# Optimization experiments

Hardware: AMD Instinct MI355X
Metric: run time of the kernel (lower is better)

Reference implementation:

```python
import jax, jax.numpy as jnp
import numpy as np
import math

B, S, D_MODEL = 2, 2048, 1024
H = 16
DK = D_MODEL // H          # 64, down-proj per-stream dim
NOPE, ROPE = 128, 64
D_HEAD = NOPE + ROPE       # 192 = d_latent // H
D_LATENT = H * D_HEAD      # 3072
ROT_DIM = 2 * ((ROPE // 2) // 2)  # rotary dim actually rotated = qk_rope_dim//2 = 32
EPS = 1e-6


def _rmsnorm(x, w):
    out = x * jax.lax.rsqrt(jnp.mean(x * x, axis=-1, keepdims=True) + EPS)
    return out * w


def _apply_rope(x):
    # x: [b, h, s, d]; rotate first ROT_DIM channels, interleaved pairing
    s = x.shape[-2]
    inv_freq = 1.0 / (10000.0 ** (jnp.arange(0, ROT_DIM, 2, dtype=jnp.float32) / ROT_DIM))
    freqs = jnp.arange(s, dtype=jnp.float32)[:, None] * inv_freq[None, :]  # [s, ROT_DIM//2]
    freqs = jnp.repeat(freqs, 2, axis=-1)  # [s, ROT_DIM], (f0,f0,f1,f1,...)
    cos, sin = jnp.cos(freqs), jnp.sin(freqs)
    xl, xr = x[..., :ROT_DIM], x[..., ROT_DIM:]
    x1, x2 = xl[..., 0::2], xl[..., 1::2]
    rot = jnp.stack([-x2, x1], axis=-1).reshape(xl.shape)
    xl = xl * cos + rot * sin
    return jnp.concatenate([xl, xr], axis=-1)


def setup_inputs() -> dict:
    key = jax.random.key(0)
    ks = jax.random.split(key, 5)
    sc = 0.02
    x = jax.random.normal(ks[0], (B, S, D_MODEL), jnp.float32)
    mask = jnp.broadcast_to(jnp.tril(jnp.ones((S, S), jnp.int32)), (B, S, S))
    w_down = jax.random.normal(ks[1], (D_MODEL, 3 * DK), jnp.float32) * sc
    rms_w = jnp.ones((3 * DK,), jnp.float32)
    w_up = jax.random.normal(ks[2], (3 * DK, 3 * D_LATENT), jnp.float32) * sc
    w_o = jax.random.normal(ks[3], (D_LATENT, D_MODEL), jnp.float32) * sc
    return {"x": x, "mask": mask, "w_down": w_down, "rms_w": rms_w, "w_up": w_up, "w_o": w_o}


def reference(x, mask, w_down, rms_w, w_up, w_o):
    h = x @ w_down                        # [b, s, 3*dk]
    h = _rmsnorm(h, rms_w)
    qkv = h @ w_up                        # [b, s, 3*d_latent]
    q, k, v = jnp.split(qkv, 3, axis=-1)  # each [b, s, d_latent]

    def to_heads(t):
        # einops '(d h)': d outer, h inner
        return t.reshape(B, S, D_HEAD, H).transpose(0, 3, 1, 2)  # [b, h, s, d]

    q, k, v = to_heads(q), to_heads(k), to_heads(v)
    q_nope, q_rope = q[..., :NOPE], q[..., NOPE:]
    k_nope, k_rope = k[..., :NOPE], k[..., NOPE:]
    q_rope = _apply_rope(q_rope)
    k_rope = _apply_rope(k_rope)

    scores = (jnp.einsum('bhid,bhjd->bhij', q_nope, k_nope)
              + jnp.einsum('bhid,bhjd->bhij', q_rope, k_rope))
    scores = scores / math.sqrt(NOPE + ROPE)
    scores = jnp.where(mask[:, None] == 0, -1e9, scores)
    attn = jax.nn.softmax(scores, axis=-1)

    out = jnp.einsum('bhij,bhjd->bhid', attn, v)        # [b, h, s, d]
    out = out.transpose(0, 2, 1, 3).reshape(B, S, D_LATENT)  # 'b h s d -> b s (h d)'
    return out @ w_o
```

## Files before the change

kernel.cpp:

```cpp
#include <hip/hip_runtime.h>
#include <stdint.h>
#include <stddef.h>


typedef __bf16 bf16x8 __attribute__((ext_vector_type(8)));
typedef float  f32x4  __attribute__((ext_vector_type(4)));

#define MFMA16x16(a,b,c) __builtin_amdgcn_mfma_f32_16x16x32_bf16((a),(b),(c),0,0,0)

__device__ __forceinline__ uint16_t f2bf(float f){
  union { float f; uint32_t u; } v; v.f = f;
  uint32_t u = v.u + 0x7fffu + ((v.u >> 16) & 1u);
  return (uint16_t)(u >> 16);
}
__device__ __forceinline__ bf16x8 load_frag(const uint16_t* p){
  uint4 u = *reinterpret_cast<const uint4*>(p);
  return __builtin_bit_cast(bf16x8, u);
}
__device__ __forceinline__ f32x4 fzero(){
  f32x4 z = {0.f, 0.f, 0.f, 0.f};
  return z;
}
__device__ __forceinline__ uint32_t pack2(float a, float b){
  return (uint32_t)f2bf(a) | ((uint32_t)f2bf(b) << 16);
}
__device__ __forceinline__ void gl2lds16(const uint16_t* g, uint16_t* l){
  __builtin_amdgcn_global_load_lds(
      (const __attribute__((address_space(1))) uint32_t*)g,
      (__attribute__((address_space(3))) uint32_t*)l,
      16, 0, 0);
}

__global__ __launch_bounds__(256) void k_transpose_cvt(const float* __restrict__ in,
                                                       uint16_t* __restrict__ out,
                                                       int R, int C){
  __shared__ float t[32][33];
  const int tc = blockIdx.x * 32;
  const int tr = blockIdx.y * 32;
  const int j = threadIdx.x & 31, i0 = threadIdx.x >> 5;
  for(int ii = 0; ii < 4; ++ii){
    int r = i0 + ii * 8;
    t[r][j] = in[(size_t)(tr + r) * C + tc + j];
  }
  __syncthreads();
  for(int ii = 0; ii < 4; ++ii){
    int c = i0 + ii * 8;
    out[(size_t)(tc + c) * R + tr + j] = f2bf(t[j][c]);
  }
}

__global__ __launch_bounds__(256) void k_down_mfma(const float* __restrict__ x,
                                                   const uint16_t* __restrict__ wdt,
                                                   const float* __restrict__ rms_w,
                                                   uint16_t* __restrict__ h_out){
  __shared__ __align__(16) uint16_t as[32 * 64];
  __shared__ float hsq[32];
  const int tid  = threadIdx.x;
  const int wave = tid >> 6, lane = tid & 63;
  const int ml = lane & 15, qd = lane >> 4;
  const int m0 = blockIdx.x * 32;
  const int n0w = wave * 48;
  if(tid < 32) hsq[tid] = 0.f;

  f32x4 acc[2][3];
#pragma unroll
  for(int mt = 0; mt < 2; ++mt)
#pragma unroll
    for(int nt = 0; nt < 3; ++nt) acc[mt][nt] = fzero();

  const int srow = tid >> 3, sc = tid & 7;
  for(int kt = 0; kt < 16; ++kt){
    const float* src = x + (size_t)(m0 + srow) * 1024 + kt * 64 + sc * 8;
    float4 a = *reinterpret_cast<const float4*>(src);
    float4 b = *reinterpret_cast<const float4*>(src + 4);
    uint4 pk;
    pk.x = pack2(a.x, a.y); pk.y = pack2(a.z, a.w);
    pk.z = pack2(b.x, b.y); pk.w = pack2(b.z, b.w);
    __syncthreads();
    *reinterpret_cast<uint4*>(as + srow * 64 + ((sc ^ (srow & 7)) * 8)) = pk;
    __syncthreads();
#pragma unroll
    for(int kk = 0; kk < 2; ++kk){
      bf16x8 af[2];
#pragma unroll
      for(int mt = 0; mt < 2; ++mt){
        int row = mt * 16 + ml;
        af[mt] = load_frag(as + row * 64 + (((kk * 4 + qd) ^ (row & 7)) * 8));
      }
#pragma unroll
      for(int nt = 0; nt < 3; ++nt){
        bf16x8 bfr = load_frag(wdt + (size_t)(n0w + nt * 16 + ml) * 1024 + kt * 64 + kk * 32 + qd * 8);
#pragma unroll
        for(int mt = 0; mt < 2; ++mt)
          acc[mt][nt] = MFMA16x16(af[mt], bfr, acc[mt][nt]);
      }
    }
  }
  __syncthreads();
#pragma unroll
  for(int mt = 0; mt < 2; ++mt)
#pragma unroll
    for(int r = 0; r < 4; ++r){
      float s = acc[mt][0][r]*acc[mt][0][r] + acc[mt][1][r]*acc[mt][1][r] + acc[mt][2][r]*acc[mt][2][r];
#pragma unroll
      for(int off = 1; off < 16; off <<= 1) s += __shfl_xor(s, off);
      if(ml == 0) atomicAdd(&hsq[mt * 16 + qd * 4 + r], s);
    }
  __syncthreads();
  float rw[3];
#pragma unroll
  for(int nt = 0; nt < 3; ++nt) rw[nt] = rms_w[n0w + nt * 16 + ml];
#pragma unroll
  for(int mt = 0; mt < 2; ++mt)
#pragma unroll
    for(int r = 0; r < 4; ++r){
      int row = mt * 16 + qd * 4 + r;
      float scl = rsqrtf(hsq[row] * (1.0f / 192.0f) + 1e-6f);
#pragma unroll
      for(int nt = 0; nt < 3; ++nt)
        h_out[(size_t)(m0 + row) * 192 + n0w + nt * 16 + ml] = f2bf(acc[mt][nt][r] * scl * rw[nt]);
    }
}

__global__ __launch_bounds__(256) void k_gemm_up(const uint16_t* __restrict__ hmat,
                                                 const uint16_t* __restrict__ wt,
                                                 uint16_t* __restrict__ q_t,
                                                 uint16_t* __restrict__ k_t,
                                                 uint16_t* __restrict__ v_t){
  __shared__ __align__(16) uint16_t rp[16 * 129 * 8];
  const int wave = threadIdx.x >> 6, lane = threadIdx.x & 63;
  const int ml = lane & 15, qd = lane >> 4;
  const int m0 = blockIdx.y * 32;
  const int bx = blockIdx.x;
  const int which = bx / 6;
  const int d0b = (bx % 6) * 32;
  const int n0w = bx * 512 + wave * 128;
  const int d0w = d0b + wave * 8;

  bf16x8 af[2][6];
#pragma unroll
  for(int mt = 0; mt < 2; ++mt)
#pragma unroll
    for(int kk = 0; kk < 6; ++kk)
      af[mt][kk] = load_frag(hmat + (size_t)(m0 + mt * 16 + ml) * 192 + kk * 32 + qd * 8);

  f32x4 acc[8][2];
#pragma unroll
  for(int nt = 0; nt < 8; ++nt){ acc[nt][0] = fzero(); acc[nt][1] = fzero(); }
#pragma unroll
  for(int nt = 0; nt < 8; ++nt){
#pragma unroll
    for(int kk = 0; kk < 6; ++kk){
      bf16x8 b = load_frag(wt + (size_t)(n0w + nt * 16 + ml) * 192 + kk * 32 + qd * 8);
      acc[nt][0] = MFMA16x16(af[0][kk], b, acc[nt][0]);
      acc[nt][1] = MFMA16x16(af[1][kk], b, acc[nt][1]);
    }
  }

  const int b   = m0 >> 11;
  const int s0  = m0 & 2047;
  const int kt2 = s0 >> 6;
  const int row0 = s0 & 63;
  uint4* rp4 = (uint4*)rp;

  if(which < 2){
    const float qs = which ? 1.0f : 0.07216878364870322f;
    const bool rope = (d0w >= 128) && (d0w < 160);
#pragma unroll
    for(int mt = 0; mt < 2; ++mt)
#pragma unroll
      for(int r = 0; r < 4; ++r){
        int t = mt * 16 + qd * 4 + r;
        int s = s0 + t;
        float v[8];
#pragma unroll
        for(int nt = 0; nt < 8; ++nt) v[nt] = acc[nt][mt][r] * qs;
        if(rope){
#pragma unroll
          for(int pi = 0; pi < 4; ++pi){
            int fi = (d0w + 2 * pi - 128) >> 1;
            float invf = __expf(-(float)fi * 0.5756462732485114f);
            float sn, cs;
            sincosf((float)s * invf, &sn, &cs);
            float e = v[2 * pi], o = v[2 * pi + 1];
            v[2 * pi]     = e * cs - o * sn;
            v[2 * pi + 1] = o * cs + e * sn;
          }
        }
        uint4 pk;
        pk.x = pack2(v[0], v[1]); pk.y = pack2(v[2], v[3]);
        pk.z = pack2(v[4], v[5]); pk.w = pack2(v[6], v[7]);
        rp4[ml * 129 + t * 4 + (wave ^ (t & 3))] = pk;
      }
  } else {
#pragma unroll
    for(int nt = 0; nt < 8; ++nt){
      int dl = wave * 8 + nt;
#pragma unroll
      for(int mt = 0; mt < 2; ++mt){
        int jc = mt * 2 + (qd >> 1);
        int slot = ml * 129 + dl * 4 + (jc ^ (dl & 3));
        uint2 pk;
        pk.x = pack2(acc[nt][mt][0], acc[nt][mt][1]);
        pk.y = pack2(acc[nt][mt][2], acc[nt][mt][3]);
        *(reinterpret_cast<uint2*>(rp + slot * 8) + (qd & 1)) = pk;
      }
    }
  }
  __syncthreads();

  if(which < 2){
    uint16_t* dst = which ? k_t : q_t;
    const int cb = d0b >> 3;
#pragma unroll
    for(int it = 0; it < 8; ++it){
      int h = wave * 4 + (it & 3), rhalf = it >> 2;
      int tloc = rhalf * 16 + (lane >> 2), p = lane & 3;
      int row = row0 + tloc;
      uint4 val = rp4[h * 129 + tloc * 4 + p];
      size_t off = ((size_t)(b * 16 + h) * 32 + kt2) * 12288
                 + (size_t)row * 192 + ((cb ^ (tloc & 4)) + p) * 8;
      *reinterpret_cast<uint4*>(dst + off) = val;
    }
  } else {
    const int cs0 = row0 >> 3;
#pragma unroll
    for(int it = 0; it < 8; ++it){
      int h = wave * 4 + (it & 3), dhalf = it >> 2;
      int dl = dhalf * 16 + (lane >> 2), p = lane & 3;
      uint4 val = rp4[h * 129 + dl * 4 + p];
      size_t off = ((size_t)(b * 16 + h) * 32 + kt2) * 12288
                 + (size_t)(d0b + dl) * 64 + ((cs0 ^ (dl & 4)) + p) * 8;
      *reinterpret_cast<uint4*>(v_t + off) = val;
    }
  }
}

__global__ __launch_bounds__(256, 4) void k_attn(const uint16_t* __restrict__ q_t,
                                                 const uint16_t* __restrict__ k_t,
                                                 const uint16_t* __restrict__ v_t,
                                                 uint16_t* __restrict__ attn_out){
  __shared__ __align__(16) uint16_t smem[15360];
  const int tid  = threadIdx.x;
  const int wave = tid >> 6;
  const int lane = tid & 63;
  const int ml   = lane & 15;
  const int qd   = lane >> 4;
  const int bx   = blockIdx.x;
  const int bh   = bx & 31;
  const int qt   = 31 - (bx >> 5);
  const int last = 2 * qt + 1;

  uint16_t* const kb  = smem;
  uint16_t* const vb  = smem + 6144;
  uint16_t* const psw = smem + 12800 + wave * 640;

  const uint16_t* kbase = k_t + (size_t)bh * 393216;
  const uint16_t* vbase = v_t + (size_t)bh * 393216;
  const uint16_t* qtile = q_t + (size_t)bh * 393216 + (size_t)qt * 12288;
  const int hh = bh & 15, bb = bh >> 4;

  const int c_  = (lane & 3) ^ ((lane >> 3) & 3);
  const int s7_ = (lane >> 2) & 7;
  const int vg_ = (lane >> 2) * 64;
  const int voff0 = vg_ + (((0 + c_) ^ s7_) * 8);
  const int voff1 = vg_ + (((4 + c_) ^ s7_) * 8);
  const int vpo = ml * 32 + ((qd ^ ((ml >> 1) & 3)) * 8);

#pragma unroll
  for(int it = 0; it < 6; ++it){
    int seg = wave * 6 + it;
    gl2lds16(qtile + seg * 512 + lane * 8, smem + seg * 512);
  }
  __builtin_amdgcn_sched_barrier(0);
  asm volatile("s_waitcnt vmcnt(0)" ::: "memory");
  __builtin_amdgcn_sched_barrier(0);
  __builtin_amdgcn_s_barrier();

  bf16x8 qf[6];
  {
    int row = wave * 16 + ml;
#pragma unroll
    for(int kk = 0; kk < 6; ++kk)
      qf[kk] = load_frag(smem + row * 192 + (((kk * 4 + qd) ^ (row & 7)) * 8));
  }
  ((uint32_t*)(vb + 6144))[tid] = 0x3F803F80u;
  asm volatile("s_waitcnt lgkmcnt(0)" ::: "memory");
  __builtin_amdgcn_sched_barrier(0);
  __builtin_amdgcn_s_barrier();

  auto stageKV = [&](int kt){
    const uint16_t* ksrc = kbase + (size_t)(kt >> 1) * 12288 + (kt & 1) * 6144
                         + wave * 1536 + lane * 8;
    uint16_t* kd = kb + wave * 1536;
    gl2lds16(ksrc,        kd);
    gl2lds16(ksrc + 512,  kd + 512);
    gl2lds16(ksrc + 1024, kd + 1024);
    const int vo = (kt & 1) ? voff1 : voff0;
    const uint16_t* vsrc = vbase + (size_t)(kt >> 1) * 12288 + (size_t)(wave * 3) * 1024 + vo;
    uint16_t* vd = vb + wave * 1536;
    gl2lds16(vsrc,        vd);
    gl2lds16(vsrc + 1024, vd + 512);
    gl2lds16(vsrc + 2048, vd + 1024);
  };

  stageKV(0);

  f32x4 o[13];
#pragma unroll
  for(int i = 0; i < 13; ++i) o[i] = fzero();

  const int r0 = qt * 64 + wave * 16;
  for(int kt = 0; kt <= last; ++kt){
    __builtin_amdgcn_sched_barrier(0);
    asm volatile("s_waitcnt vmcnt(0)" ::: "memory");
    __builtin_amdgcn_sched_barrier(0);
    __builtin_amdgcn_s_barrier();

    const int kl = kt * 32;
    if(kl <= r0 + 15){
      float pp[2][4];
      __builtin_amdgcn_s_setprio(1);
#pragma unroll
      for(int nt = 0; nt < 2; ++nt){
        f32x4 a = fzero();
        int row = nt * 16 + ml;
#pragma unroll
        for(int kk = 0; kk < 6; ++kk){
          bf16x8 bfr = load_frag(kb + row * 192 + (((kk * 4 + qd) ^ (row & 7)) * 8));
          a = MFMA16x16(qf[kk], bfr, a);
        }
#pragma unroll
        for(int r = 0; r < 4; ++r) pp[nt][r] = a[r];
      }
      __builtin_amdgcn_s_setprio(0);
      const bool diag = (kl + 31 > r0);
#pragma unroll
      for(int nt = 0; nt < 2; ++nt)
#pragma unroll
        for(int r = 0; r < 4; ++r){
          float v = pp[nt][r];
          if(diag){
            int i = r0 + qd * 4 + r;
            int j = kl + nt * 16 + ml;
            if(j > i) v = -1e9f;
          }
          pp[nt][r] = __expf(v);
        }
#pragma unroll
      for(int nt = 0; nt < 2; ++nt)
#pragma unroll
        for(int r = 0; r < 4; ++r)
          psw[(qd * 4 + r) * 40 + nt * 16 + ml] = f2bf(pp[nt][r]);
      bf16x8 pa = load_frag(psw + ml * 40 + qd * 8);
      __builtin_amdgcn_s_setprio(1);
#pragma unroll
      for(int dt = 0; dt < 13; ++dt){
        bf16x8 vbf = load_frag(vb + dt * 512 + vpo);
        o[dt] = MFMA16x16(pa, vbf, o[dt]);
      }
      __builtin_amdgcn_s_setprio(0);
    }
    __builtin_amdgcn_s_barrier();
    if(kt < last) stageKV(kt + 1);
  }

#pragma unroll
  for(int r = 0; r < 4; ++r){
    int i = r0 + qd * 4 + r;
    float inv = 1.0f / o[12][r];
    size_t obase = ((size_t)bb * 2048 + i) * 3072 + hh * 192;
#pragma unroll
    for(int dt = 0; dt < 12; ++dt)
      attn_out[obase + dt * 16 + ml] = f2bf(o[dt][r] * inv);
  }
}

__global__ __launch_bounds__(256) void k_gemm_o_tile(const uint16_t* __restrict__ a,
                                                     const uint16_t* __restrict__ wt,
                                                     float* __restrict__ part){
  __shared__ __align__(16) uint16_t as[128 * 64];
  __shared__ __align__(16) uint16_t bs[128 * 64];
  const int wave = threadIdx.x >> 6, lane = threadIdx.x & 63;
  const int ml = lane & 15, qd = lane >> 4;
  const int m0 = blockIdx.y * 128, n0 = blockIdx.x * 128;
  const int kz = blockIdx.z;
  const int mo = (wave >> 1) * 64, no = (wave & 1) * 64;

  const int lrow = lane >> 3;
  const int gch  = (lane & 7) ^ (lrow & 7);
  const uint16_t* abase = a  + (size_t)(m0 + lrow) * 3072 + kz * 1536 + gch * 8;
  const uint16_t* bbase = wt + (size_t)(n0 + lrow) * 3072 + kz * 1536 + gch * 8;

  f32x4 acc[4][4];
#pragma unroll
  for(int mt = 0; mt < 4; ++mt)
#pragma unroll
    for(int nt = 0; nt < 4; ++nt) acc[mt][nt] = fzero();

  for(int kt = 0; kt < 24; ++kt){
    __syncthreads();
#pragma unroll
    for(int it = 0; it < 4; ++it){
      int seg = it * 4 + wave;
      gl2lds16(abase + (size_t)seg * 24576 + kt * 64, as + seg * 512);
      gl2lds16(bbase + (size_t)seg * 24576 + kt * 64, bs + seg * 512);
    }
    __syncthreads();
#pragma unroll
    for(int ks2 = 0; ks2 < 2; ++ks2){
      bf16x8 af[4], bfr[4];
#pragma unroll
      for(int mt = 0; mt < 4; ++mt){
        int row = mo + mt * 16 + ml;
        af[mt] = load_frag(as + row * 64 + (((ks2 * 4 + qd) ^ (row & 7)) * 8));
      }
#pragma unroll
      for(int nt = 0; nt < 4; ++nt){
        int row = no + nt * 16 + ml;
        bfr[nt] = load_frag(bs + row * 64 + (((ks2 * 4 + qd) ^ (row & 7)) * 8));
      }
#pragma unroll
      for(int mt = 0; mt < 4; ++mt)
#pragma unroll
        for(int nt = 0; nt < 4; ++nt)
          acc[mt][nt] = MFMA16x16(af[mt], bfr[nt], acc[mt][nt]);
    }
  }

  float* dst = part + (size_t)kz * 4096 * 1024;
#pragma unroll
  for(int mt = 0; mt < 4; ++mt)
#pragma unroll
    for(int nt = 0; nt < 4; ++nt)
#pragma unroll
      for(int r = 0; r < 4; ++r){
        int row = m0 + mo + mt * 16 + qd * 4 + r;
        int col = n0 + no + nt * 16 + ml;
        dst[(size_t)row * 1024 + col] = acc[mt][nt][r];
      }
}

__global__ __launch_bounds__(256) void k_addout(const float* __restrict__ part,
                                                float* __restrict__ out){
  int i = blockIdx.x * 256 + threadIdx.x;
  const float4* p0 = (const float4*)part;
  const float4* p1 = p0 + (size_t)1048576;
  float4 a = p0[i], b = p1[i];
  float4 c; c.x = a.x + b.x; c.y = a.y + b.y; c.z = a.z + b.z; c.w = a.w + b.w;
  ((float4*)out)[i] = c;
}


extern "C" void kernel_launch(void* const* d_in, const int* in_sizes, int n_in,
                              void* d_out, int out_size, void* d_ws, size_t ws_size,
                              hipStream_t stream) {
  (void)in_sizes; (void)n_in; (void)out_size; (void)ws_size;
  const float* x      = (const float*)d_in[0];
  const float* w_down = (const float*)d_in[2];
  const float* rms_w  = (const float*)d_in[3];
  const float* w_up   = (const float*)d_in[4];
  const float* w_o    = (const float*)d_in[5];
  float* out = (float*)d_out;

  char* ws = (char*)d_ws;
  uint16_t* h_bf   = (uint16_t*)(ws);
  uint16_t* w_up_t = (uint16_t*)(ws + 1572864);
  uint16_t* w_o_t  = (uint16_t*)(ws + 5111808);
  uint16_t* w_dn_t = (uint16_t*)(ws + 11403264);
  uint16_t* q_tb   = (uint16_t*)(ws + 11796480);
  uint16_t* k_tb   = (uint16_t*)(ws + 36962304);
  uint16_t* v_tb   = (uint16_t*)(ws + 62128128);
  uint16_t* attnO  = (uint16_t*)(ws + 87293952);
  float*    part   = (float*)(ws + 11796480);

  k_transpose_cvt<<<dim3(288, 6), 256, 0, stream>>>(w_up, w_up_t, 192, 9216);
  k_transpose_cvt<<<dim3(32, 96), 256, 0, stream>>>(w_o,  w_o_t,  3072, 1024);
  k_transpose_cvt<<<dim3(6, 32),  256, 0, stream>>>(w_down, w_dn_t, 1024, 192);
  k_down_mfma<<<128, 256, 0, stream>>>(x, w_dn_t, rms_w, h_bf);
  k_gemm_up<<<dim3(18, 128), 256, 0, stream>>>(h_bf, w_up_t, q_tb, k_tb, v_tb);
  k_attn<<<1024, 256, 0, stream>>>(q_tb, k_tb, v_tb, attnO);
  k_gemm_o_tile<<<dim3(8, 32, 2), 256, 0, stream>>>(attnO, w_o_t, part);
  k_addout<<<4096, 256, 0, stream>>>(part, out);
}
```

Before: 350.2 us.

## Process two query tiles per attention block with double-buffered K/V staging

Each attention block now handles 128 query rows (two 64-row tiles) instead of 64, so every K/V tile staged into LDS feeds both Q tiles and K/V global traffic is halved. K/V buffers are double-buffered so the next tile's load is issued before computing on the current one, overlapping memory with MFMA work. Q fragments are loaded straight from global into registers, and blocks are ordered to pair heavy and light causal rows. In exchange, register use roughly doubles for accumulators (occupancy hint lowered to 2 blocks), grid size halves to 512 blocks, and LDS use doubles.

New measurement: 375.1 us. 1.07x slower.

```diff
diff --git a/kernel.cpp b/kernel.cpp
--- a/kernel.cpp
+++ b/kernel.cpp
@@ -236,11 +236,11 @@
   }
 }
 
-__global__ __launch_bounds__(256, 4) void k_attn(const uint16_t* __restrict__ q_t,
+__global__ __launch_bounds__(256, 2) void k_attn(const uint16_t* __restrict__ q_t,
                                                  const uint16_t* __restrict__ k_t,
                                                  const uint16_t* __restrict__ v_t,
                                                  uint16_t* __restrict__ attn_out){
-  __shared__ __align__(16) uint16_t smem[15360];
+  __shared__ __align__(16) uint16_t smem[30720];
   const int tid  = threadIdx.x;
   const int wave = tid >> 6;
   const int lane = tid & 63;
@@ -248,131 +248,150 @@
   const int qd   = lane >> 4;
   const int bx   = blockIdx.x;
   const int bh   = bx & 31;
-  const int qt   = 31 - (bx >> 5);
-  const int last = 2 * qt + 1;
-
-  uint16_t* const kb  = smem;
-  uint16_t* const vb  = smem + 6144;
-  uint16_t* const psw = smem + 12800 + wave * 640;
+  const int qb   = (bx < 256) ? (15 - (bx >> 5)) : ((bx >> 5) - 8);
+  const int last = 4 * qb + 3;
+
+  uint16_t* const kb0 = smem;
+  uint16_t* const kb1 = smem + 6144;
+  uint16_t* const vb0 = smem + 12288;
+  uint16_t* const vb1 = smem + 18944;
+  uint16_t* const psw = smem + 25600 + wave * 1280;
 
   const uint16_t* kbase = k_t + (size_t)bh * 393216;
   const uint16_t* vbase = v_t + (size_t)bh * 393216;
-  const uint16_t* qtile = q_t + (size_t)bh * 393216 + (size_t)qt * 12288;
   const int hh = bh & 15, bb = bh >> 4;
 
   const int c_  = (lane & 3) ^ ((lane >> 3) & 3);
   const int s7_ = (lane >> 2) & 7;
   const int vg_ = (lane >> 2) * 64;
-  const int voff0 = vg_ + (((0 + c_) ^ s7_) * 8);
+  const int voff0 = vg_ + ((c_ ^ s7_) * 8);
   const int voff1 = vg_ + (((4 + c_) ^ s7_) * 8);
   const int vpo = ml * 32 + ((qd ^ ((ml >> 1) & 3)) * 8);
 
-#pragma unroll
-  for(int it = 0; it < 6; ++it){
-    int seg = wave * 6 + it;
-    gl2lds16(qtile + seg * 512 + lane * 8, smem + seg * 512);
+  bf16x8 qf[2][6];
+  {
+    const int row = wave * 16 + ml;
+    const int sw = row & 7;
+#pragma unroll
+    for(int t = 0; t < 2; ++t){
+      const uint16_t* qtb = q_t + ((size_t)bh * 32 + qb * 2 + t) * 12288 + (size_t)row * 192;
+#pragma unroll
+      for(int kk = 0; kk < 6; ++kk)
+        qf[t][kk] = load_frag(qtb + (((kk * 4 + qd) ^ sw) * 8));
+    }
   }
   __builtin_amdgcn_sched_barrier(0);
   asm volatile("s_waitcnt vmcnt(0)" ::: "memory");
   __builtin_amdgcn_sched_barrier(0);
-  __builtin_amdgcn_s_barrier();
-
-  bf16x8 qf[6];
-  {
-    int row = wave * 16 + ml;
-#pragma unroll
-    for(int kk = 0; kk < 6; ++kk)
-      qf[kk] = load_frag(smem + row * 192 + (((kk * 4 + qd) ^ (row & 7)) * 8));
-  }
-  ((uint32_t*)(vb + 6144))[tid] = 0x3F803F80u;
-  asm volatile("s_waitcnt lgkmcnt(0)" ::: "memory");
-  __builtin_amdgcn_sched_barrier(0);
-  __builtin_amdgcn_s_barrier();
-
-  auto stageKV = [&](int kt){
+
+  ((uint32_t*)(vb0 + 6144))[tid] = 0x3F803F80u;
+  ((uint32_t*)(vb1 + 6144))[tid] = 0x3F803F80u;
+
+  auto stageKV = [&](int kt, int sel){
     const uint16_t* ksrc = kbase + (size_t)(kt >> 1) * 12288 + (kt & 1) * 6144
                          + wave * 1536 + lane * 8;
-    uint16_t* kd = kb + wave * 1536;
+    uint16_t* kd = (sel ? kb1 : kb0) + wave * 1536;
     gl2lds16(ksrc,        kd);
     gl2lds16(ksrc + 512,  kd + 512);
     gl2lds16(ksrc + 1024, kd + 1024);
     const int vo = (kt & 1) ? voff1 : voff0;
     const uint16_t* vsrc = vbase + (size_t)(kt >> 1) * 12288 + (size_t)(wave * 3) * 1024 + vo;
-    uint16_t* vd = vb + wave * 1536;
+    uint16_t* vd = (sel ? vb1 : vb0) + wave * 1536;
     gl2lds16(vsrc,        vd);
     gl2lds16(vsrc + 1024, vd + 512);
     gl2lds16(vsrc + 2048, vd + 1024);
   };
 
-  stageKV(0);
-
-  f32x4 o[13];
-#pragma unroll
-  for(int i = 0; i < 13; ++i) o[i] = fzero();
-
-  const int r0 = qt * 64 + wave * 16;
+  stageKV(0, 0);
+  asm volatile("s_waitcnt lgkmcnt(0)" ::: "memory");
+
+  f32x4 o[2][13];
+#pragma unroll
+  for(int t = 0; t < 2; ++t)
+#pragma unroll
+    for(int i = 0; i < 13; ++i) o[t][i] = fzero();
+
+  const int r0 = qb * 128 + wave * 16;
+  const int r1 = r0 + 64;
+  int cur = 0;
   for(int kt = 0; kt <= last; ++kt){
-    __builtin_amdgcn_sched_barrier(0);
-    asm volatile("s_waitcnt vmcnt(0)" ::: "memory");
-    __builtin_amdgcn_sched_barrier(0);
+    if(kt < last){
+      stageKV(kt + 1, cur ^ 1);
+      __builtin_amdgcn_sched_barrier(0);
+      asm volatile("s_waitcnt vmcnt(6)" ::: "memory");
+      __builtin_amdgcn_sched_barrier(0);
+    } else {
+      asm volatile("s_waitcnt vmcnt(0)" ::: "memory");
+      __builtin_amdgcn_sched_barrier(0);
+    }
     __builtin_amdgcn_s_barrier();
 
     const int kl = kt * 32;
-    if(kl <= r0 + 15){
-      float pp[2][4];
+    if(kl <= r1 + 15){
+      const uint16_t* kc = cur ? kb1 : kb0;
+      const uint16_t* vc = cur ? vb1 : vb0;
+      const bool a0 = (kl <= r0 + 15);
+
+      f32x4 s[2][2];
+      s[0][0] = fzero(); s[0][1] = fzero(); s[1][0] = fzero(); s[1][1] = fzero();
       __builtin_amdgcn_s_setprio(1);
 #pragma unroll
       for(int nt = 0; nt < 2; ++nt){
-        f32x4 a = fzero();
         int row = nt * 16 + ml;
 #pragma unroll
         for(int kk = 0; kk < 6; ++kk){
-          bf16x8 bfr = load_frag(kb + row * 192 + (((kk * 4 + qd) ^ (row & 7)) * 8));
-          a = MFMA16x16(qf[kk], bfr, a);
+          bf16x8 bfr = load_frag(kc + row * 192 + (((kk * 4 + qd) ^ (row & 7)) * 8));
+          if(a0) s[0][nt] = MFMA16x16(qf[0][kk], bfr, s[0][nt]);
+          s[1][nt] = MFMA16x16(qf[1][kk], bfr, s[1][nt]);
         }
-#pragma unroll
-        for(int r = 0; r < 4; ++r) pp[nt][r] = a[r];
       }
       __builtin_amdgcn_s_setprio(0);
-      const bool diag = (kl + 31 > r0);
-#pragma unroll
-      for(int nt = 0; nt < 2; ++nt)
-#pragma unroll
-        for(int r = 0; r < 4; ++r){
-          float v = pp[nt][r];
-          if(diag){
-            int i = r0 + qd * 4 + r;
-            int j = kl + nt * 16 + ml;
-            if(j > i) v = -1e9f;
+
+#pragma unroll
+      for(int t = 0; t < 2; ++t){
+        if(t == 0 && !a0) continue;
+        const int rq = t ? r1 : r0;
+        const bool diag = (kl + 31 > rq);
+#pragma unroll
+        for(int nt = 0; nt < 2; ++nt)
+#pragma unroll
+          for(int r = 0; r < 4; ++r){
+            float v = s[t][nt][r];
+            if(diag){
+              int i = rq + qd * 4 + r;
+              int j = kl + nt * 16 + ml;
+              if(j > i) v = -1e9f;
+            }
+            psw[(t * 16 + qd * 4 + r) * 40 + nt * 16 + ml] = f2bf(__expf(v));
           }
-          pp[nt][r] = __expf(v);
-        }
-#pragma unroll
-      for(int nt = 0; nt < 2; ++nt)
-#pragma unroll
-        for(int r = 0; r < 4; ++r)
-          psw[(qd * 4 + r) * 40 + nt * 16 + ml] = f2bf(pp[nt][r]);
-      bf16x8 pa = load_frag(psw + ml * 40 + qd * 8);
+      }
+      bf16x8 pa0 = load_frag(psw + ml * 40 + qd * 8);
+      bf16x8 pa1 = load_frag(psw + (16 + ml) * 40 + qd * 8);
       __builtin_amdgcn_s_setprio(1);
 #pragma unroll
       for(int dt = 0; dt < 13; ++dt){
-        bf16x8 vbf = load_frag(vb + dt * 512 + vpo);
-        o[dt] = MFMA16x16(pa, vbf, o[dt]);
+        bf16x8 vbf = load_frag(vc + dt * 512 + vpo);
+        if(a0) o[0][dt] = MFMA16x16(pa0, vbf, o[0][dt]);
+        o[1][dt] = MFMA16x16(pa1, vbf, o[1][dt]);
       }
       __builtin_amdgcn_s_setprio(0);
     }
     __builtin_amdgcn_s_barrier();
-    if(kt < last) stageKV(kt + 1);
-  }
-
-#pragma unroll
-  for(int r = 0; r < 4; ++r){
-    int i = r0 + qd * 4 + r;
-    float inv = 1.0f / o[12][r];
-    size_t obase = ((size_t)bb * 2048 + i) * 3072 + hh * 192;
-#pragma unroll
-    for(int dt = 0; dt < 12; ++dt)
-      attn_out[obase + dt * 16 + ml] = f2bf(o[dt][r] * inv);
+    cur ^= 1;
+  }
+
+#pragma unroll
+  for(int t = 0; t < 2; ++t){
+    const int rq = t ? r1 : r0;
+#pragma unroll
+    for(int r = 0; r < 4; ++r){
+      int i = rq + qd * 4 + r;
+      float inv = 1.0f / o[t][12][r];
+      size_t obase = ((size_t)bb * 2048 + i) * 3072 + hh * 192;
+#pragma unroll
+      for(int dt = 0; dt < 12; ++dt)
+        attn_out[obase + dt * 16 + ml] = f2bf(o[t][dt][r] * inv);
+    }
   }
 }
 
@@ -479,7 +498,7 @@
   k_transpose_cvt<<<dim3(6, 32),  256, 0, stream>>>(w_down, w_dn_t, 1024, 192);
   k_down_mfma<<<128, 256, 0, stream>>>(x, w_dn_t, rms_w, h_bf);
   k_gemm_up<<<dim3(18, 128), 256, 0, stream>>>(h_bf, w_up_t, q_tb, k_tb, v_tb);
-  k_attn<<<1024, 256, 0, stream>>>(q_tb, k_tb, v_tb, attnO);
+  k_attn<<<512, 256, 0, stream>>>(q_tb, k_tb, v_tb, attnO);
   k_gemm_o_tile<<<dim3(8, 32, 2), 256, 0, stream>>>(attnO, w_o_t, part);
   k_addout<<<4096, 256, 0, stream>>>(part, out);
 }
```
